# Optimization experiments

Hardware: AMD Instinct MI355X
Metric: run time of the kernel (lower is better)

Reference implementation:

```python
import jax, jax.numpy as jnp
import numpy as np

N = 50000            # nodes (cells)
E_RAND = 1_600_000   # random edges; self loops appended -> E = E_RAND + N
DIMS = [(512, 384), (384, 256), (256, 128)]  # (in, hidden) per encoder stage
OUT = 128


def setup_inputs() -> dict:
    key = jax.random.key(0)
    ks = jax.random.split(key, 16)
    features = jax.random.normal(ks[0], (N, DIMS[0][0]), dtype=jnp.float32)
    src = jax.random.randint(ks[1], (E_RAND,), 0, N, dtype=jnp.int32)
    dst = jax.random.randint(ks[2], (E_RAND,), 0, N, dtype=jnp.int32)
    loops = jnp.arange(N, dtype=jnp.int32)  # dgl.add_self_loop
    src = jnp.concatenate([src, loops])
    dst = jnp.concatenate([dst, loops])
    inp = {"features": features, "src": src, "dst": dst}
    i = 3
    for s, (din, dout) in enumerate(DIMS):
        inp[f"sage_w{s}"] = jax.random.normal(ks[i], (dout, din), jnp.float32) / np.sqrt(din); i += 1
        inp[f"sage_b{s}"] = jnp.zeros((dout,), jnp.float32)
        inp[f"gc_w{s}"] = jax.random.normal(ks[i], (dout, dout), jnp.float32) / np.sqrt(dout); i += 1
        inp[f"gc_b{s}"] = jnp.zeros((dout,), jnp.float32)
    inp["fc_w"] = jax.random.normal(ks[i], (OUT, DIMS[-1][1]), jnp.float32) / np.sqrt(DIMS[-1][1])
    inp["fc_b"] = jnp.zeros((OUT,), jnp.float32)
    return inp


def reference(features, src, dst,
              sage_w0, sage_b0, gc_w0, gc_b0,
              sage_w1, sage_b1, gc_w1, gc_b1,
              sage_w2, sage_b2, gc_w2, gc_b2,
              fc_w, fc_b):
    ones = jnp.ones((src.shape[0],), jnp.float32)
    in_deg = jax.ops.segment_sum(ones, dst, num_segments=N)
    out_deg = jax.ops.segment_sum(ones, src, num_segments=N)
    # GraphConv norm='both' scalers (clamp degree to >=1, as DGL does)
    inv_src = jnp.where(out_deg > 0, out_deg, 1.0) ** -0.5  # [N]
    inv_dst = jnp.where(in_deg > 0, in_deg, 1.0) ** -0.5    # [N]
    sage_den = (in_deg + 1.0)[:, None]                      # SAGE 'gcn' denominator

    def sage_gcn(h, w, b):
        # DGL SAGEConv aggregator_type='gcn': (sum_neigh + self)/(in_deg+1) -> fc_neigh
        agg = jax.ops.segment_sum(h[src], dst, num_segments=N)
        return ((agg + h) / sage_den) @ w.T + b

    def graph_conv(h, w, b):
        # DGL GraphConv norm='both': D_out^{-1/2} -> sum aggregate -> D_in^{-1/2} -> W
        hn = h * inv_src[:, None]
        agg = jax.ops.segment_sum(hn[src], dst, num_segments=N)
        return (agg * inv_dst[:, None]) @ w.T + b

    params = [(sage_w0, sage_b0, gc_w0, gc_b0),
              (sage_w1, sage_b1, gc_w1, gc_b1),
              (sage_w2, sage_b2, gc_w2, gc_b2)]
    h = features
    for sw, sb, gw, gb in params:
        h = jax.nn.relu(sage_gcn(h, sw, sb))
        h = jax.nn.relu(graph_conv(h, gw, gb))
    return h @ fc_w.T + fc_b
```

## Files before the change

### kernel.cpp

```cpp
#include <hip/hip_runtime.h>
#include <cstddef>
#include <cstdint>


typedef _Float16 h8 __attribute__((ext_vector_type(8)));
typedef _Float16 h4 __attribute__((ext_vector_type(4)));
typedef float f32x4 __attribute__((ext_vector_type(4)));


__global__ __launch_bounds__(256) void deg_kernel(
    const int* __restrict__ src, const int* __restrict__ dst,
    int* __restrict__ in_deg, int* __restrict__ out_deg, int E) {
  int e = blockIdx.x * 256 + threadIdx.x;
  if (e < E) {
    atomicAdd(&in_deg[dst[e]], 1);
    atomicAdd(&out_deg[src[e]], 1);
  }
}

__global__ __launch_bounds__(1024) void scan_kernel(
    const int* __restrict__ deg, int* __restrict__ row_ptr, int n) {
  __shared__ int buf[1024];
  __shared__ int carry_s;
  if (threadIdx.x == 0) carry_s = 0;
  __syncthreads();
  for (int base = 0; base < n; base += 1024) {
    int i = base + (int)threadIdx.x;
    int v = (i < n) ? deg[i] : 0;
    buf[threadIdx.x] = v;
    __syncthreads();
    #pragma unroll
    for (int off = 1; off < 1024; off <<= 1) {
      int t = 0;
      if ((int)threadIdx.x >= off) t = buf[threadIdx.x - off];
      __syncthreads();
      buf[threadIdx.x] += t;
      __syncthreads();
    }
    int incl  = buf[threadIdx.x];
    int carry = carry_s;
    int total = buf[1023];
    __syncthreads();
    if (i < n) row_ptr[i] = carry + incl - v;
    if (threadIdx.x == 0) carry_s = carry + total;
    __syncthreads();
  }
  if (threadIdx.x == 0) row_ptr[n] = carry_s;
}

__global__ __launch_bounds__(256) void scatter_kernel(
    const int* __restrict__ src, const int* __restrict__ dst,
    const int* __restrict__ row_ptr, int* __restrict__ cnt,
    int* __restrict__ csr, int E) {
  int e = blockIdx.x * 256 + threadIdx.x;
  if (e < E) {
    int d = dst[e];
    int pos = row_ptr[d] + atomicAdd(&cnt[d], 1);
    csr[pos] = src[e];
  }
}

__global__ __launch_bounds__(256) void scaler_kernel(
    const int* __restrict__ in_deg, const int* __restrict__ out_deg,
    float* __restrict__ inv_src, float* __restrict__ inv_dst,
    float* __restrict__ inv_den, int n) {
  int i = blockIdx.x * 256 + threadIdx.x;
  if (i < n) {
    float od = (float)out_deg[i];
    float id = (float)in_deg[i];
    inv_src[i] = rsqrtf(od > 0.f ? od : 1.0f);
    inv_dst[i] = rsqrtf(id > 0.f ? id : 1.0f);
    inv_den[i] = 1.0f / (id + 1.0f);
  }
}


__global__ __launch_bounds__(256) void cvt_kernel(
    const float* __restrict__ in, _Float16* __restrict__ out,
    long n_in, long n_pad) {
  long i = ((long)blockIdx.x * 256 + (long)threadIdx.x) * 4;
  if (i >= n_pad) return;
  float4 v = (i < n_in) ? *(const float4*)(in + i) : make_float4(0.f, 0.f, 0.f, 0.f);
  h4 h = {(_Float16)v.x, (_Float16)v.y, (_Float16)v.z, (_Float16)v.w};
  *(h4*)(out + i) = h;
}


template <typename OutT>
__global__ __launch_bounds__(256) void hgemm(
    const _Float16* __restrict__ A, const _Float16* __restrict__ W,
    OutT* __restrict__ C, int Mstore, int K, int Nc,
    const float* __restrict__ row_scale, const float* __restrict__ bias) {
  __shared__ _Float16 As[128 * 32];
  __shared__ _Float16 Bs[128 * 32];
  const int tid = threadIdx.x;
  const int bm = blockIdx.x * 128, bn = blockIdx.y * 128;
  const int wave = tid >> 6, lane = tid & 63;
  const int wm = (wave & 1) * 64, wn = (wave >> 1) * 64;
  const int lrow = lane & 15, lq = lane >> 4;

  const int r0 = tid >> 2;
  const int cc = (tid & 3) * 8;
  const _Float16* Ag = A + (size_t)(bm + r0) * K + cc;
  const _Float16* Wg = W + (size_t)(bn + r0) * K + cc;
  const size_t rs64 = (size_t)64 * K;

  f32x4 acc[4][4];
  #pragma unroll
  for (int i = 0; i < 4; ++i)
    #pragma unroll
    for (int j = 0; j < 4; ++j) acc[i][j] = (f32x4){0.f, 0.f, 0.f, 0.f};

  for (int k0 = 0; k0 < K; k0 += 32) {
    uint4 a0 = *(const uint4*)(Ag + k0);
    uint4 a1 = *(const uint4*)(Ag + rs64 + k0);
    uint4 b0 = *(const uint4*)(Wg + k0);
    uint4 b1 = *(const uint4*)(Wg + rs64 + k0);
    __syncthreads();
    *(uint4*)(As + r0 * 32 + cc) = a0;
    *(uint4*)(As + (64 + r0) * 32 + cc) = a1;
    *(uint4*)(Bs + r0 * 32 + cc) = b0;
    *(uint4*)(Bs + (64 + r0) * 32 + cc) = b1;
    __syncthreads();
    h8 af[4], bf[4];
    #pragma unroll
    for (int i = 0; i < 4; ++i)
      af[i] = *(const h8*)(As + (wm + i * 16 + lrow) * 32 + lq * 8);
    #pragma unroll
    for (int j = 0; j < 4; ++j)
      bf[j] = *(const h8*)(Bs + (wn + j * 16 + lrow) * 32 + lq * 8);
    #pragma unroll
    for (int i = 0; i < 4; ++i)
      #pragma unroll
      for (int j = 0; j < 4; ++j)
        acc[i][j] = __builtin_amdgcn_mfma_f32_16x16x32_f16(af[i], bf[j], acc[i][j], 0, 0, 0);
  }

  #pragma unroll
  for (int i = 0; i < 4; ++i) {
    #pragma unroll
    for (int r = 0; r < 4; ++r) {
      const int m = bm + wm + i * 16 + lq * 4 + r;
      if (m < Mstore) {
        const float rsc = row_scale ? row_scale[m] : 1.0f;
        OutT* crow = C + (size_t)m * Nc + bn + wn + lrow;
        #pragma unroll
        for (int j = 0; j < 4; ++j) {
          float v = acc[i][j][r] * rsc;
          if (bias) v += bias[bn + wn + j * 16 + lrow];
          crow[j * 16] = (OutT)v;
        }
      }
    }
  }
}


template <int D, bool SELF>
__global__ __launch_bounds__(256) void agg_h(
    const _Float16* __restrict__ Z, const int* __restrict__ row_ptr,
    const int* __restrict__ csr, const float* __restrict__ out_scale,
    const float* __restrict__ bias, _Float16* __restrict__ out, int n) {
  constexpr int CH = D / 8;
  constexpr int GROUP = 16;
  constexpr int NV = CH / GROUP;
  const int gid = threadIdx.x >> 4;
  const int lane = threadIdx.x & 15;
  const int node = blockIdx.x * 16 + gid;
  if (node >= n) return;

  const int rs = row_ptr[node], re = row_ptr[node + 1];

  float acc[NV][8];
  #pragma unroll
  for (int v = 0; v < NV; ++v)
    #pragma unroll
    for (int q = 0; q < 8; ++q) acc[v][q] = 0.f;

  for (int e = rs; e < re; e += GROUP) {
    int m = re - e; if (m > GROUP) m = GROUP;
    int eid = (lane < m) ? csr[e + lane] : 0;
    for (int j = 0; j < m; ++j) {
      int s = __shfl(eid, j, GROUP);
      const h8* zr = (const h8*)(Z + (size_t)s * D);
      #pragma unroll
      for (int v = 0; v < NV; ++v) {
        h8 t = zr[lane + v * GROUP];
        #pragma unroll
        for (int q = 0; q < 8; ++q) acc[v][q] += (float)t[q];
      }
    }
  }

  const float osc = out_scale[node];
  const h8* zs = (const h8*)(Z + (size_t)node * D);
  _Float16* orow = out + (size_t)node * D;
  #pragma unroll
  for (int v = 0; v < NV; ++v) {
    const int idx = lane + v * GROUP;
    if (SELF) {
      h8 t = zs[idx];
      #pragma unroll
      for (int q = 0; q < 8; ++q) acc[v][q] += (float)t[q];
    }
    h8 r;
    #pragma unroll
    for (int q = 0; q < 8; ++q) {
      float x = acc[v][q] * osc + bias[idx * 8 + q];
      r[q] = (_Float16)fmaxf(x, 0.f);
    }
    *(h8*)(orow + idx * 8) = r;
  }
}


static void launch_cvt(const float* in, _Float16* out, long n_in, long n_pad,
                       hipStream_t st) {
  long thr = n_pad / 4;
  cvt_kernel<<<(int)((thr + 255) / 256), 256, 0, st>>>(in, out, n_in, n_pad);
}

extern "C" void kernel_launch(void* const* d_in, const int* in_sizes, int n_in,
                              void* d_out, int out_size, void* d_ws, size_t ws_size,
                              hipStream_t stream) {
  const float* features = (const float*)d_in[0];
  const int*   src      = (const int*)d_in[1];
  const int*   dst      = (const int*)d_in[2];
  const float* wsrc[7] = {(const float*)d_in[3],  (const float*)d_in[5],
                          (const float*)d_in[7],  (const float*)d_in[9],
                          (const float*)d_in[11], (const float*)d_in[13],
                          (const float*)d_in[15]};
  const float* sb[3] = {(const float*)d_in[4],  (const float*)d_in[8],  (const float*)d_in[12]};
  const float* gb[3] = {(const float*)d_in[6],  (const float*)d_in[10], (const float*)d_in[14]};
  const float* fc_b  = (const float*)d_in[16];

  const int N = in_sizes[0] / 512;
  const int E = in_sizes[1];
  const int MB = (N + 127) / 128;
  const int Mpad = MB * 128;

  const int wcnt[7] = {384 * 512, 384 * 384, 256 * 384, 256 * 256,
                       128 * 256, 128 * 128, 128 * 128};

  char* ws = (char*)d_ws;
  _Float16* featH = (_Float16*)ws;
  _Float16* hA    = featH + (size_t)Mpad * 512;
  _Float16* hB    = hA + (size_t)Mpad * 384;
  _Float16* wH[7];
  {
    _Float16* p = hB + (size_t)Mpad * 384;
    for (int i = 0; i < 7; ++i) { wH[i] = p; p += wcnt[i]; }
  }
  int* csr     = (int*)(wH[6] + wcnt[6]);
  int* rp      = csr + E;
  int* in_dg   = rp + (N + 1);
  int* out_dg  = in_dg + N;
  int* cnt     = out_dg + N;
  float* inv_src = (float*)(cnt + N);
  float* inv_dst = inv_src + N;
  float* inv_den = inv_dst + N;

  size_t totw = 0; for (int i = 0; i < 7; ++i) totw += wcnt[i];
  size_t needed = ((size_t)Mpad * (512 + 384 + 384) + totw) * 2 +
                  ((size_t)E + (N + 1) + 6 * (size_t)N) * 4;
  if (ws_size < needed) return;

  (void)hipMemsetAsync(in_dg, 0, sizeof(int) * 3 * (size_t)N, stream);

  const int eb = (E + 255) / 256;
  const int nb = (N + 255) / 256;
  deg_kernel<<<eb, 256, 0, stream>>>(src, dst, in_dg, out_dg, E);
  scan_kernel<<<1, 1024, 0, stream>>>(in_dg, rp, N);
  scatter_kernel<<<eb, 256, 0, stream>>>(src, dst, rp, cnt, csr, E);
  scaler_kernel<<<nb, 256, 0, stream>>>(in_dg, out_dg, inv_src, inv_dst, inv_den, N);

  launch_cvt(features, featH, (long)N * 512, (long)Mpad * 512, stream);
  for (int i = 0; i < 7; ++i) launch_cvt(wsrc[i], wH[i], wcnt[i], wcnt[i], stream);

  const int dout[3] = {384, 256, 128};
  const _Float16* h = featH;
  int K = 512;
  for (int s = 0; s < 3; ++s) {
    const int D = dout[s];
    dim3 gg(MB, D / 128);
    const int ab = (N + 15) / 16;
    hgemm<_Float16><<<gg, 256, 0, stream>>>(h, wH[2 * s], hB, Mpad, K, D, nullptr, nullptr);
    if (D == 384)      agg_h<384, true><<<ab, 256, 0, stream>>>(hB, rp, csr, inv_den, sb[s], hA, N);
    else if (D == 256) agg_h<256, true><<<ab, 256, 0, stream>>>(hB, rp, csr, inv_den, sb[s], hA, N);
    else               agg_h<128, true><<<ab, 256, 0, stream>>>(hB, rp, csr, inv_den, sb[s], hA, N);
    hgemm<_Float16><<<gg, 256, 0, stream>>>(hA, wH[2 * s + 1], hB, Mpad, D, D, inv_src, nullptr);
    if (D == 384)      agg_h<384, false><<<ab, 256, 0, stream>>>(hB, rp, csr, inv_dst, gb[s], hA, N);
    else if (D == 256) agg_h<256, false><<<ab, 256, 0, stream>>>(hB, rp, csr, inv_dst, gb[s], hA, N);
    else               agg_h<128, false><<<ab, 256, 0, stream>>>(hB, rp, csr, inv_dst, gb[s], hA, N);
    h = hA;
    K = D;
  }
  dim3 gf(MB, 1);
  hgemm<float><<<gf, 256, 0, stream>>>(h, wH[6], (float*)d_out, N, 128, 128, nullptr, fc_b);
}
```

Before: 1.371 ms.

## Use direct global-to-LDS loads in GEMM and batch four edge gathers in aggregation

The GEMM tile loads now go straight from global memory into LDS through global_load_lds, so the data no longer passes through registers and separate LDS stores. The aggregation kernel now issues four neighbor-row gathers before accumulating any of them, which keeps more loads in flight per lane to hide gather latency. The unroll adds register pressure in the aggregation kernel. The direct-to-LDS path also depends on how lanes map to LDS addresses; here the per-thread offset tid*8 matches the old row-major layout.

New measurement: 1.356 ms. About the same (-1.1%).

```diff
diff --git a/kernel.cpp b/kernel.cpp
--- a/kernel.cpp
+++ b/kernel.cpp
@@ -83,6 +83,13 @@
   float4 v = (i < n_in) ? *(const float4*)(in + i) : make_float4(0.f, 0.f, 0.f, 0.f);
   h4 h = {(_Float16)v.x, (_Float16)v.y, (_Float16)v.z, (_Float16)v.w};
   *(h4*)(out + i) = h;
+}
+
+
+__device__ __forceinline__ void gload_lds16(const _Float16* g, _Float16* l) {
+  __builtin_amdgcn_global_load_lds(
+      (const __attribute__((address_space(1))) void*)g,
+      (__attribute__((address_space(3))) void*)l, 16, 0, 0);
 }
 
 
@@ -104,6 +111,10 @@
   const _Float16* Ag = A + (size_t)(bm + r0) * K + cc;
   const _Float16* Wg = W + (size_t)(bn + r0) * K + cc;
   const size_t rs64 = (size_t)64 * K;
+  _Float16* As0 = As + tid * 8;
+  _Float16* As1 = As + 64 * 32 + tid * 8;
+  _Float16* Bs0 = Bs + tid * 8;
+  _Float16* Bs1 = Bs + 64 * 32 + tid * 8;
 
   f32x4 acc[4][4];
   #pragma unroll
@@ -112,15 +123,11 @@
     for (int j = 0; j < 4; ++j) acc[i][j] = (f32x4){0.f, 0.f, 0.f, 0.f};
 
   for (int k0 = 0; k0 < K; k0 += 32) {
-    uint4 a0 = *(const uint4*)(Ag + k0);
-    uint4 a1 = *(const uint4*)(Ag + rs64 + k0);
-    uint4 b0 = *(const uint4*)(Wg + k0);
-    uint4 b1 = *(const uint4*)(Wg + rs64 + k0);
-    __syncthreads();
-    *(uint4*)(As + r0 * 32 + cc) = a0;
-    *(uint4*)(As + (64 + r0) * 32 + cc) = a1;
-    *(uint4*)(Bs + r0 * 32 + cc) = b0;
-    *(uint4*)(Bs + (64 + r0) * 32 + cc) = b1;
+    __syncthreads();
+    gload_lds16(Ag + k0, As0);
+    gload_lds16(Ag + rs64 + k0, As1);
+    gload_lds16(Wg + k0, Bs0);
+    gload_lds16(Wg + rs64 + k0, Bs1);
     __syncthreads();
     h8 af[4], bf[4];
     #pragma unroll
@@ -156,14 +163,54 @@
 }
 
 
+template <int D>
+__device__ __forceinline__ void acc_edges4(
+    float (*acc)[8], const _Float16* __restrict__ Z, int lane,
+    int s0, int s1, int s2, int s3, int k) {
+  constexpr int NV = D / 128;
+  const h8* z0 = (const h8*)(Z + (size_t)s0 * D) + lane;
+  const h8* z1 = (const h8*)(Z + (size_t)s1 * D) + lane;
+  const h8* z2 = (const h8*)(Z + (size_t)s2 * D) + lane;
+  const h8* z3 = (const h8*)(Z + (size_t)s3 * D) + lane;
+  h8 t0[NV], t1[NV], t2[NV], t3[NV];
+  #pragma unroll
+  for (int v = 0; v < NV; ++v) t0[v] = z0[v * 16];
+  #pragma unroll
+  for (int v = 0; v < NV; ++v) t1[v] = z1[v * 16];
+  #pragma unroll
+  for (int v = 0; v < NV; ++v) t2[v] = z2[v * 16];
+  #pragma unroll
+  for (int v = 0; v < NV; ++v) t3[v] = z3[v * 16];
+  #pragma unroll
+  for (int v = 0; v < NV; ++v)
+    #pragma unroll
+    for (int q = 0; q < 8; ++q) acc[v][q] += (float)t0[v][q];
+  if (k > 1) {
+    #pragma unroll
+    for (int v = 0; v < NV; ++v)
+      #pragma unroll
+      for (int q = 0; q < 8; ++q) acc[v][q] += (float)t1[v][q];
+  }
+  if (k > 2) {
+    #pragma unroll
+    for (int v = 0; v < NV; ++v)
+      #pragma unroll
+      for (int q = 0; q < 8; ++q) acc[v][q] += (float)t2[v][q];
+  }
+  if (k > 3) {
+    #pragma unroll
+    for (int v = 0; v < NV; ++v)
+      #pragma unroll
+      for (int q = 0; q < 8; ++q) acc[v][q] += (float)t3[v][q];
+  }
+}
+
 template <int D, bool SELF>
 __global__ __launch_bounds__(256) void agg_h(
     const _Float16* __restrict__ Z, const int* __restrict__ row_ptr,
     const int* __restrict__ csr, const float* __restrict__ out_scale,
     const float* __restrict__ bias, _Float16* __restrict__ out, int n) {
-  constexpr int CH = D / 8;
-  constexpr int GROUP = 16;
-  constexpr int NV = CH / GROUP;
+  constexpr int NV = D / 128;
   const int gid = threadIdx.x >> 4;
   const int lane = threadIdx.x & 15;
   const int node = blockIdx.x * 16 + gid;
@@ -177,18 +224,19 @@
     #pragma unroll
     for (int q = 0; q < 8; ++q) acc[v][q] = 0.f;
 
-  for (int e = rs; e < re; e += GROUP) {
-    int m = re - e; if (m > GROUP) m = GROUP;
-    int eid = (lane < m) ? csr[e + lane] : 0;
-    for (int j = 0; j < m; ++j) {
-      int s = __shfl(eid, j, GROUP);
-      const h8* zr = (const h8*)(Z + (size_t)s * D);
-      #pragma unroll
-      for (int v = 0; v < NV; ++v) {
-        h8 t = zr[lane + v * GROUP];
-        #pragma unroll
-        for (int q = 0; q < 8; ++q) acc[v][q] += (float)t[q];
-      }
+  for (int e = rs; e < re; e += 16) {
+    int m = re - e; if (m > 16) m = 16;
+    const int eid = (lane < m) ? csr[e + lane] : 0;
+    #pragma unroll 1
+    for (int j = 0; j < m; j += 4) {
+      const int i1 = (j + 1 < m) ? j + 1 : m - 1;
+      const int i2 = (j + 2 < m) ? j + 2 : m - 1;
+      const int i3 = (j + 3 < m) ? j + 3 : m - 1;
+      const int s0 = __shfl(eid, j, 16);
+      const int s1 = __shfl(eid, i1, 16);
+      const int s2 = __shfl(eid, i2, 16);
+      const int s3 = __shfl(eid, i3, 16);
+      acc_edges4<D>(acc, Z, lane, s0, s1, s2, s3, m - j);
     }
   }
 
@@ -197,7 +245,7 @@
   _Float16* orow = out + (size_t)node * D;
   #pragma unroll
   for (int v = 0; v < NV; ++v) {
-    const int idx = lane + v * GROUP;
+    const int idx = lane + v * 16;
     if (SELF) {
       h8 t = zs[idx];
       #pragma unroll
```

## Write GEMM outputs in 32-column panels and aggregate panel by panel

Applied to the files above, without the earlier changes.

The GEMM epilogue now writes intermediate outputs in a panel-major layout of 32-column slices, and aggregation runs as one launch per panel. Each launch gathers 64-byte panel rows, so the gathered working set (N×64B, about 3.2MB) can stay in cache, where the full gathered matrix could not. The GEMM also switches to direct global-to-LDS loads, and the aggregation uses nontemporal CSR loads and output stores. The cost is many more kernel launches, CSR indices re-read for every panel, and strided, less coalesced GEMM stores.

After: 1.966 ms. 43.4% more time.

```diff
diff --git a/kernel.cpp b/kernel.cpp
--- a/kernel.cpp
+++ b/kernel.cpp
@@ -86,11 +86,19 @@
 }
 
 
+__device__ __forceinline__ void gload_lds16(const _Float16* g, _Float16* l) {
+  __builtin_amdgcn_global_load_lds(
+      (const __attribute__((address_space(1))) void*)g,
+      (__attribute__((address_space(3))) void*)l, 16, 0, 0);
+}
+
+
 template <typename OutT>
 __global__ __launch_bounds__(256) void hgemm(
     const _Float16* __restrict__ A, const _Float16* __restrict__ W,
     OutT* __restrict__ C, int Mstore, int K, int Nc,
-    const float* __restrict__ row_scale, const float* __restrict__ bias) {
+    const float* __restrict__ row_scale, const float* __restrict__ bias,
+    size_t pstride) {
   __shared__ _Float16 As[128 * 32];
   __shared__ _Float16 Bs[128 * 32];
   const int tid = threadIdx.x;
@@ -104,6 +112,10 @@
   const _Float16* Ag = A + (size_t)(bm + r0) * K + cc;
   const _Float16* Wg = W + (size_t)(bn + r0) * K + cc;
   const size_t rs64 = (size_t)64 * K;
+  _Float16* As0 = As + tid * 8;
+  _Float16* As1 = As + 64 * 32 + tid * 8;
+  _Float16* Bs0 = Bs + tid * 8;
+  _Float16* Bs1 = Bs + 64 * 32 + tid * 8;
 
   f32x4 acc[4][4];
   #pragma unroll
@@ -112,15 +124,11 @@
     for (int j = 0; j < 4; ++j) acc[i][j] = (f32x4){0.f, 0.f, 0.f, 0.f};
 
   for (int k0 = 0; k0 < K; k0 += 32) {
-    uint4 a0 = *(const uint4*)(Ag + k0);
-    uint4 a1 = *(const uint4*)(Ag + rs64 + k0);
-    uint4 b0 = *(const uint4*)(Wg + k0);
-    uint4 b1 = *(const uint4*)(Wg + rs64 + k0);
-    __syncthreads();
-    *(uint4*)(As + r0 * 32 + cc) = a0;
-    *(uint4*)(As + (64 + r0) * 32 + cc) = a1;
-    *(uint4*)(Bs + r0 * 32 + cc) = b0;
-    *(uint4*)(Bs + (64 + r0) * 32 + cc) = b1;
+    __syncthreads();
+    gload_lds16(Ag + k0, As0);
+    gload_lds16(Ag + rs64 + k0, As1);
+    gload_lds16(Wg + k0, Bs0);
+    gload_lds16(Wg + rs64 + k0, Bs1);
     __syncthreads();
     h8 af[4], bf[4];
     #pragma unroll
@@ -143,12 +151,15 @@
       const int m = bm + wm + i * 16 + lq * 4 + r;
       if (m < Mstore) {
         const float rsc = row_scale ? row_scale[m] : 1.0f;
-        OutT* crow = C + (size_t)m * Nc + bn + wn + lrow;
         #pragma unroll
         for (int j = 0; j < 4; ++j) {
+          const int c = bn + wn + j * 16 + lrow;
           float v = acc[i][j][r] * rsc;
-          if (bias) v += bias[bn + wn + j * 16 + lrow];
-          crow[j * 16] = (OutT)v;
+          if (bias) v += bias[c];
+          const size_t off = pstride
+              ? ((size_t)(c >> 5) * pstride + (size_t)m * 32 + (size_t)(c & 31))
+              : ((size_t)m * Nc + (size_t)c);
+          C[off] = (OutT)v;
         }
       }
     }
@@ -156,61 +167,68 @@
 }
 
 
-template <int D, bool SELF>
-__global__ __launch_bounds__(256) void agg_h(
-    const _Float16* __restrict__ Z, const int* __restrict__ row_ptr,
+template <bool SELF>
+__global__ __launch_bounds__(256) void agg_panel(
+    const _Float16* __restrict__ Zpm, const int* __restrict__ row_ptr,
     const int* __restrict__ csr, const float* __restrict__ out_scale,
-    const float* __restrict__ bias, _Float16* __restrict__ out, int n) {
-  constexpr int CH = D / 8;
-  constexpr int GROUP = 16;
-  constexpr int NV = CH / GROUP;
-  const int gid = threadIdx.x >> 4;
-  const int lane = threadIdx.x & 15;
-  const int node = blockIdx.x * 16 + gid;
+    const float* __restrict__ bias, _Float16* __restrict__ out,
+    int n, int Mpad, int D, int panel) {
+  const int gq = threadIdx.x >> 2;
+  const int l4 = threadIdx.x & 3;
+  const int node = blockIdx.x * 64 + gq;
   if (node >= n) return;
 
+  const _Float16* Zp = Zpm + (size_t)panel * (size_t)Mpad * 32 + (size_t)l4 * 8;
   const int rs = row_ptr[node], re = row_ptr[node + 1];
 
-  float acc[NV][8];
+  float acc[8];
   #pragma unroll
-  for (int v = 0; v < NV; ++v)
-    #pragma unroll
-    for (int q = 0; q < 8; ++q) acc[v][q] = 0.f;
-
-  for (int e = rs; e < re; e += GROUP) {
-    int m = re - e; if (m > GROUP) m = GROUP;
-    int eid = (lane < m) ? csr[e + lane] : 0;
-    for (int j = 0; j < m; ++j) {
-      int s = __shfl(eid, j, GROUP);
-      const h8* zr = (const h8*)(Z + (size_t)s * D);
+  for (int q = 0; q < 8; ++q) acc[q] = 0.f;
+
+  for (int e = rs; e < re; e += 4) {
+    int idx = e + l4;
+    if (idx >= re) idx = re - 1;
+    const int eid = __builtin_nontemporal_load(csr + idx);
+    const int s0 = __shfl(eid, 0, 4);
+    const int s1 = __shfl(eid, 1, 4);
+    const int s2 = __shfl(eid, 2, 4);
+    const int s3 = __shfl(eid, 3, 4);
+    h8 t0 = *(const h8*)(Zp + (size_t)s0 * 32);
+    h8 t1 = *(const h8*)(Zp + (size_t)s1 * 32);
+    h8 t2 = *(const h8*)(Zp + (size_t)s2 * 32);
+    h8 t3 = *(const h8*)(Zp + (size_t)s3 * 32);
+    const int nrem = re - e;
+    #pragma unroll
+    for (int q = 0; q < 8; ++q) acc[q] += (float)t0[q];
+    if (nrem > 1) {
       #pragma unroll
-      for (int v = 0; v < NV; ++v) {
-        h8 t = zr[lane + v * GROUP];
-        #pragma unroll
-        for (int q = 0; q < 8; ++q) acc[v][q] += (float)t[q];
-      }
-    }
+      for (int q = 0; q < 8; ++q) acc[q] += (float)t1[q];
+    }
+    if (nrem > 2) {
+      #pragma unroll
+      for (int q = 0; q < 8; ++q) acc[q] += (float)t2[q];
+    }
+    if (nrem > 3) {
+      #pragma unroll
+      for (int q = 0; q < 8; ++q) acc[q] += (float)t3[q];
+    }
+  }
+
+  if (SELF) {
+    h8 ts = *(const h8*)(Zp + (size_t)node * 32);
+    #pragma unroll
+    for (int q = 0; q < 8; ++q) acc[q] += (float)ts[q];
   }
 
   const float osc = out_scale[node];
-  const h8* zs = (const h8*)(Z + (size_t)node * D);
-  _Float16* orow = out + (size_t)node * D;
+  const int c0 = panel * 32 + l4 * 8;
+  h8 r;
   #pragma unroll
-  for (int v = 0; v < NV; ++v) {
-    const int idx = lane + v * GROUP;
-    if (SELF) {
-      h8 t = zs[idx];
-      #pragma unroll
-      for (int q = 0; q < 8; ++q) acc[v][q] += (float)t[q];
-    }
-    h8 r;
-    #pragma unroll
-    for (int q = 0; q < 8; ++q) {
-      float x = acc[v][q] * osc + bias[idx * 8 + q];
-      r[q] = (_Float16)fmaxf(x, 0.f);
-    }
-    *(h8*)(orow + idx * 8) = r;
-  }
+  for (int q = 0; q < 8; ++q) {
+    float x = acc[q] * osc + bias[c0 + q];
+    r[q] = (_Float16)fmaxf(x, 0.f);
+  }
+  __builtin_nontemporal_store(r, (h8*)(out + (size_t)node * D + c0));
 }
 
 
@@ -277,24 +295,28 @@
   launch_cvt(features, featH, (long)N * 512, (long)Mpad * 512, stream);
   for (int i = 0; i < 7; ++i) launch_cvt(wsrc[i], wH[i], wcnt[i], wcnt[i], stream);
 
+  const size_t pstride = (size_t)Mpad * 32;
   const int dout[3] = {384, 256, 128};
   const _Float16* h = featH;
   int K = 512;
   for (int s = 0; s < 3; ++s) {
     const int D = dout[s];
     dim3 gg(MB, D / 128);
-    const int ab = (N + 15) / 16;
-    hgemm<_Float16><<<gg, 256, 0, stream>>>(h, wH[2 * s], hB, Mpad, K, D, nullptr, nullptr);
-    if (D == 384)      agg_h<384, true><<<ab, 256, 0, stream>>>(hB, rp, csr, inv_den, sb[s], hA, N);
-    else if (D == 256) agg_h<256, true><<<ab, 256, 0, stream>>>(hB, rp, csr, inv_den, sb[s], hA, N);
-    else               agg_h<128, true><<<ab, 256, 0, stream>>>(hB, rp, csr, inv_den, sb[s], hA, N);
-    hgemm<_Float16><<<gg, 256, 0, stream>>>(hA, wH[2 * s + 1], hB, Mpad, D, D, inv_src, nullptr);
-    if (D == 384)      agg_h<384, false><<<ab, 256, 0, stream>>>(hB, rp, csr, inv_dst, gb[s], hA, N);
-    else if (D == 256) agg_h<256, false><<<ab, 256, 0, stream>>>(hB, rp, csr, inv_dst, gb[s], hA, N);
-    else               agg_h<128, false><<<ab, 256, 0, stream>>>(hB, rp, csr, inv_dst, gb[s], hA, N);
+    const int ab = (N + 63) / 64;
+    hgemm<_Float16><<<gg, 256, 0, stream>>>(h, wH[2 * s], hB, Mpad, K, D,
+                                            nullptr, nullptr, pstride);
+    for (int p = 0; p < D / 32; ++p)
+      agg_panel<true><<<ab, 256, 0, stream>>>(hB, rp, csr, inv_den, sb[s], hA,
+                                              N, Mpad, D, p);
+    hgemm<_Float16><<<gg, 256, 0, stream>>>(hA, wH[2 * s + 1], hB, Mpad, D, D,
+                                            inv_src, nullptr, pstride);
+    for (int p = 0; p < D / 32; ++p)
+      agg_panel<false><<<ab, 256, 0, stream>>>(hB, rp, csr, inv_dst, gb[s], hA,
+                                               N, Mpad, D, p);
     h = hA;
     K = D;
   }
   dim3 gf(MB, 1);
-  hgemm<float><<<gf, 256, 0, stream>>>(h, wH[6], (float*)d_out, N, 128, 128, nullptr, fc_b);
-}
+  hgemm<float><<<gf, 256, 0, stream>>>(h, wH[6], (float*)d_out, N, 128, 128,
+                                       nullptr, fc_b, 0);
+}
```
